# Kernel optimization log

Measured on AMD Instinct MI355X. Metric: run time of the kernel, lower is better.

## Reference

```python
import jax, jax.numpy as jnp
import numpy as np

BS, N, C = 16, 128, 512
EPS = 1e-5


def setup_inputs() -> dict:
    key = jax.random.key(0)
    ks = jax.random.split(key, 6)
    x = jax.random.normal(ks[0], (BS, N, C), dtype=jnp.float32)
    y = jax.random.normal(ks[1], (BS, C), dtype=jnp.float32)
    # edge conv: Conv2d(2C -> 1, 1x1), init std sqrt(2/(1*1*1))
    conv_e_w = jax.random.normal(ks[2], (1, 2 * C), dtype=jnp.float32) * np.sqrt(2.0)
    conv_e_b = jnp.zeros((1,), dtype=jnp.float32)
    bn_e_g = jnp.ones((1,), dtype=jnp.float32)
    bn_e_b = jnp.zeros((1,), dtype=jnp.float32)
    bn_e_m = jnp.zeros((1,), dtype=jnp.float32)
    bn_e_v = jnp.ones((1,), dtype=jnp.float32)
    # feature conv: Conv2d(2C -> C, 1x1), init std sqrt(2/C)
    conv_f_w = jax.random.normal(ks[3], (C, 2 * C), dtype=jnp.float32) * np.sqrt(2.0 / C)
    conv_f_b = jnp.zeros((C,), dtype=jnp.float32)
    bn_f_g = jnp.ones((C,), dtype=jnp.float32)
    bn_f_b = jnp.zeros((C,), dtype=jnp.float32)
    bn_f_m = jnp.zeros((C,), dtype=jnp.float32)
    bn_f_v = jnp.ones((C,), dtype=jnp.float32)
    return {
        "x": x, "y": y,
        "conv_e_w": conv_e_w, "conv_e_b": conv_e_b,
        "bn_e_g": bn_e_g, "bn_e_b": bn_e_b, "bn_e_m": bn_e_m, "bn_e_v": bn_e_v,
        "conv_f_w": conv_f_w, "conv_f_b": conv_f_b,
        "bn_f_g": bn_f_g, "bn_f_b": bn_f_b, "bn_f_m": bn_f_m, "bn_f_v": bn_f_v,
    }


def reference(x, y, conv_e_w, conv_e_b, bn_e_g, bn_e_b, bn_e_m, bn_e_v,
              conv_f_w, conv_f_b, bn_f_g, bn_f_b, bn_f_m, bn_f_v):
    bs, n, c = x.shape
    # ---- Wcompute: pairwise |x_i - x_j| -> conv1x1(2C->1) + BN + mask + softmax ----
    diff = jnp.abs(x[:, :, None, :] - x[:, None, :, :])  # [bs, N, N, C]
    w_diff = conv_e_w[0, :c]   # weights on pairwise-diff channels
    w_y = conv_e_w[0, c:]      # weights on broadcast y channels
    # 1x1 conv collapses to einsum; y part is constant over (i, j)
    score = (jnp.einsum('bijc,c->bij', diff, w_diff)
             + (y @ w_y)[:, None, None] + conv_e_b[0])  # [bs, N, N]
    # BatchNorm2d(1), inference mode
    score = (score - bn_e_m[0]) * (bn_e_g[0] * jax.lax.rsqrt(bn_e_v[0] + EPS)) + bn_e_b[0]
    # mask diagonal (W_id * 1e8) then softmax over neighbors j
    score = score - jnp.eye(n, dtype=score.dtype)[None] * 1e8
    W = jax.nn.softmax(score, axis=2)  # [bs, N, N]
    # ---- Gconv: neighbor aggregation + conv1x1(2C->C) + BN + ReLU ----
    x_nb = jnp.einsum('bij,bjc->bic', W, x)       # [bs, N, C]
    h = jnp.concatenate([x, x_nb], axis=2)        # [bs, N, 2C]
    out = jnp.einsum('bnk,ck->bnc', h, conv_f_w) + conv_f_b  # [bs, N, C]
    # BatchNorm2d(C), inference mode (per-channel)
    out = (out - bn_f_m) * (bn_f_g * jax.lax.rsqrt(bn_f_v + EPS)) + bn_f_b
    return jax.nn.relu(out)
```

## Files before the change

### kernel.cpp

```cpp
#include <hip/hip_runtime.h>
#include <hip/hip_bf16.h>

#define NTOK 128
#define CHN  512
#define KTOT 1024
#define EPSV 1e-5f

typedef __attribute__((ext_vector_type(8))) short bf16x8;
typedef __attribute__((ext_vector_type(4))) float f32x4;

union BfPack4 { ushort4 u; __hip_bfloat16 h[4]; };


__global__ __launch_bounds__(256)
void k0_transpose(const float* __restrict__ xg,
                  float* __restrict__ xT,
                  __hip_bfloat16* __restrict__ xTbf,
                  __hip_bfloat16* __restrict__ hb)
{
    __shared__ float ts[64 * 68];
    const int t  = threadIdx.x;
    const int bk = blockIdx.x;
    const int b  = bk >> 4;
    const int jt = (bk >> 3) & 1;
    const int ct = bk & 7;
    const int j0 = jt * 64, c0 = ct * 64;

    const int jr = t >> 2, qd = t & 3;
    const float* src = xg + ((size_t)(b * NTOK) + j0 + jr) * CHN + c0 + qd * 16;
    float4 v0 = *(const float4*)&src[0];
    float4 v1 = *(const float4*)&src[4];
    float4 v2 = *(const float4*)&src[8];
    float4 v3 = *(const float4*)&src[12];
    *(float4*)&ts[jr * 68 + qd * 16 + 0]  = v0;
    *(float4*)&ts[jr * 68 + qd * 16 + 4]  = v1;
    *(float4*)&ts[jr * 68 + qd * 16 + 8]  = v2;
    *(float4*)&ts[jr * 68 + qd * 16 + 12] = v3;

    {
        __hip_bfloat16* hrow = hb + ((size_t)(b * NTOK) + j0 + jr) * KTOT + c0 + qd * 16;
        BfPack4 p;
        p.h[0]=__float2bfloat16(v0.x); p.h[1]=__float2bfloat16(v0.y);
        p.h[2]=__float2bfloat16(v0.z); p.h[3]=__float2bfloat16(v0.w);
        *(ushort4*)&hrow[0] = p.u;
        p.h[0]=__float2bfloat16(v1.x); p.h[1]=__float2bfloat16(v1.y);
        p.h[2]=__float2bfloat16(v1.z); p.h[3]=__float2bfloat16(v1.w);
        *(ushort4*)&hrow[4] = p.u;
        p.h[0]=__float2bfloat16(v2.x); p.h[1]=__float2bfloat16(v2.y);
        p.h[2]=__float2bfloat16(v2.z); p.h[3]=__float2bfloat16(v2.w);
        *(ushort4*)&hrow[8] = p.u;
        p.h[0]=__float2bfloat16(v3.x); p.h[1]=__float2bfloat16(v3.y);
        p.h[2]=__float2bfloat16(v3.z); p.h[3]=__float2bfloat16(v3.w);
        *(ushort4*)&hrow[12] = p.u;
    }
    __syncthreads();

    const int cs = t >> 4, jj = (t & 15) * 4;
    #pragma unroll
    for (int m = 0; m < 4; ++m) {
        const int c = cs + 16 * m;
        float4 o;
        o.x = ts[(jj + 0) * 68 + c];
        o.y = ts[(jj + 1) * 68 + c];
        o.z = ts[(jj + 2) * 68 + c];
        o.w = ts[(jj + 3) * 68 + c];
        const size_t base = ((size_t)(b * CHN) + c0 + c) * NTOK + j0 + jj;
        *(float4*)&xT[base] = o;
        BfPack4 p;
        p.h[0]=__float2bfloat16(o.x); p.h[1]=__float2bfloat16(o.y);
        p.h[2]=__float2bfloat16(o.z); p.h[3]=__float2bfloat16(o.w);
        *(ushort4*)&xTbf[base] = p.u;
    }
}

__global__ __launch_bounds__(128)
void k1a_scores(const float* __restrict__ xg,
                const float* __restrict__ xT,
                const float* __restrict__ wde,
                float* __restrict__ part)
{
    const int bk = blockIdx.x;
    const int s  = bk & 7;
    const int iq = (bk >> 3) & 31;
    const int b  = bk >> 8;
    const int i0 = iq * 4;
    const int c0 = s * 64;
    const int j  = threadIdx.x;

    const float* xtp = xT + ((size_t)(b * CHN) + c0) * NTOK + j;
    const float* xip = xg + ((size_t)(b * NTOK) + i0) * CHN + c0;

    float acc0 = 0.f, acc1 = 0.f, acc2 = 0.f, acc3 = 0.f;

    #pragma unroll 2
    for (int cc = 0; cc < 64; cc += 8) {
        float xj[8];
        #pragma unroll
        for (int k = 0; k < 8; ++k) xj[k] = xtp[(cc + k) * NTOK];
        #pragma unroll
        for (int k = 0; k < 8; ++k) {
            const int c = cc + k;
            const float wd  = wde[c0 + c];
            const float xi0 = xip[0 * CHN + c];
            const float xi1 = xip[1 * CHN + c];
            const float xi2 = xip[2 * CHN + c];
            const float xi3 = xip[3 * CHN + c];
            acc0 += fabsf(xi0 - xj[k]) * wd;
            acc1 += fabsf(xi1 - xj[k]) * wd;
            acc2 += fabsf(xi2 - xj[k]) * wd;
            acc3 += fabsf(xi3 - xj[k]) * wd;
        }
    }

    float* pp = part + ((size_t)s * 16 + b) * (NTOK * NTOK) + (size_t)i0 * NTOK + j;
    pp[0 * NTOK] = acc0;
    pp[1 * NTOK] = acc1;
    pp[2 * NTOK] = acc2;
    pp[3 * NTOK] = acc3;
}

__global__ __launch_bounds__(128)
void k1b_softmax(const float* __restrict__ part,
                 const float* __restrict__ bn_e_g,
                 const float* __restrict__ bn_e_v,
                 __hip_bfloat16* __restrict__ Wbf)
{
    const int bk = blockIdx.x;
    const int b  = bk >> 6;
    const int i  = (bk & 63) * 2 + (threadIdx.x >> 6);
    const int l  = threadIdx.x & 63;

    const float* pp = part + (size_t)(b * NTOK + i) * NTOK;
    float p1 = 0.f, p2 = 0.f;
    #pragma unroll
    for (int s = 0; s < 8; ++s) {
        p1 += pp[(size_t)s * 16 * NTOK * NTOK + l];
        p2 += pp[(size_t)s * 16 * NTOK * NTOK + l + 64];
    }
    const float sc = bn_e_g[0] * rsqrtf(bn_e_v[0] + EPSV);
    float l1 = p1 * sc - (l == i ? 1e8f : 0.f);
    float l2 = p2 * sc - (l + 64 == i ? 1e8f : 0.f);

    float m = fmaxf(l1, l2);
    #pragma unroll
    for (int off = 32; off > 0; off >>= 1) m = fmaxf(m, __shfl_xor(m, off));
    const float e1 = __expf(l1 - m);
    const float e2 = __expf(l2 - m);
    float ssum = e1 + e2;
    #pragma unroll
    for (int off = 32; off > 0; off >>= 1) ssum += __shfl_xor(ssum, off);
    const float inv = 1.f / ssum;

    __hip_bfloat16* wr = Wbf + (size_t)(b * NTOK + i) * NTOK;
    wr[l]      = __float2bfloat16(e1 * inv);
    wr[l + 64] = __float2bfloat16(e2 * inv);
}

__global__ __launch_bounds__(256)
void k1c_xnb(const __hip_bfloat16* __restrict__ Wbf,
             const __hip_bfloat16* __restrict__ xTbf,
             const float* __restrict__ wf,
             __hip_bfloat16* __restrict__ hb,
             __hip_bfloat16* __restrict__ wfb)
{
    const int bk = blockIdx.x;
    const int t  = threadIdx.x;

    {
        const float* wr = wf + (size_t)bk * KTOT;
        float4 u = *(const float4*)&wr[t * 4];
        BfPack4 p;
        p.h[0]=__float2bfloat16(u.x); p.h[1]=__float2bfloat16(u.y);
        p.h[2]=__float2bfloat16(u.z); p.h[3]=__float2bfloat16(u.w);
        *(ushort4*)&wfb[(size_t)bk * KTOT + t * 4] = p.u;
    }

    const int b  = bk >> 5;
    const int mt = (bk >> 3) & 3;
    const int ct = bk & 7;
    const int i0 = mt * 32, c0 = ct * 64;

    const int w    = t >> 6;
    const int lane = t & 63;
    const int wm   = w & 1;
    const int wn   = w >> 1;
    const int m16  = lane & 15;
    const int q    = lane >> 4;

    const short* A0 = (const short*)Wbf  + (size_t)(b * NTOK + i0 + wm * 16 + m16) * NTOK + q * 8;
    const short* B0 = (const short*)xTbf + ((size_t)(b * CHN) + c0 + wn * 32 + m16) * NTOK + q * 8;

    f32x4 acc0 = {0.f, 0.f, 0.f, 0.f};
    f32x4 acc1 = acc0;

    #pragma unroll
    for (int k0 = 0; k0 < NTOK; k0 += 32) {
        const bf16x8 a  = *(const bf16x8*)(A0 + k0);
        const bf16x8 b0 = *(const bf16x8*)(B0 + k0);
        const bf16x8 b1 = *(const bf16x8*)(B0 + 16 * NTOK + k0);
        acc0 = __builtin_amdgcn_mfma_f32_16x16x32_bf16(a, b0, acc0, 0, 0, 0);
        acc1 = __builtin_amdgcn_mfma_f32_16x16x32_bf16(a, b1, acc1, 0, 0, 0);
    }

    #pragma unroll
    for (int ni = 0; ni < 2; ++ni) {
        const int c = c0 + wn * 32 + ni * 16 + m16;
        const f32x4 ac = ni ? acc1 : acc0;
        #pragma unroll
        for (int r = 0; r < 4; ++r) {
            const int i = i0 + wm * 16 + q * 4 + r;
            hb[(size_t)(b * NTOK + i) * KTOT + CHN + c] = __float2bfloat16(ac[r]);
        }
    }
}

__global__ __launch_bounds__(256)
void k2_gemm_bn_relu(const __hip_bfloat16* __restrict__ hbp,
                     const __hip_bfloat16* __restrict__ wfbp,
                     const float* __restrict__ fb,
                     const float* __restrict__ gg,
                     const float* __restrict__ bb,
                     const float* __restrict__ mm,
                     const float* __restrict__ vv,
                     float* __restrict__ out)
{
    const int blk  = blockIdx.x;
    const int r0   = (blk >> 3) << 6;
    const int c0   = (blk & 7) << 6;
    const int t    = threadIdx.x;
    const int w    = t >> 6;
    const int lane = t & 63;
    const int wm   = w & 1;
    const int wn   = w >> 1;
    const int m16  = lane & 15;
    const int qq   = lane >> 4;

    const short* A0 = (const short*)hbp  + (size_t)(r0 + wm * 32 + m16) * KTOT + qq * 8;
    const short* B0 = (const short*)wfbp + (size_t)(c0 + wn * 32 + m16) * KTOT + qq * 8;

    f32x4 acc00 = {0.f, 0.f, 0.f, 0.f};
    f32x4 acc01 = acc00, acc10 = acc00, acc11 = acc00;

    #pragma unroll 4
    for (int k0 = 0; k0 < KTOT; k0 += 32) {
        const bf16x8 aA = *(const bf16x8*)(A0 + k0);
        const bf16x8 aB = *(const bf16x8*)(A0 + 16 * KTOT + k0);
        const bf16x8 bA = *(const bf16x8*)(B0 + k0);
        const bf16x8 bB = *(const bf16x8*)(B0 + 16 * KTOT + k0);
        acc00 = __builtin_amdgcn_mfma_f32_16x16x32_bf16(aA, bA, acc00, 0, 0, 0);
        acc01 = __builtin_amdgcn_mfma_f32_16x16x32_bf16(aA, bB, acc01, 0, 0, 0);
        acc10 = __builtin_amdgcn_mfma_f32_16x16x32_bf16(aB, bA, acc10, 0, 0, 0);
        acc11 = __builtin_amdgcn_mfma_f32_16x16x32_bf16(aB, bB, acc11, 0, 0, 0);
    }

    #pragma unroll
    for (int ni = 0; ni < 2; ++ni) {
        const int c = c0 + wn * 32 + ni * 16 + m16;
        const float gf = gg[c] * rsqrtf(vv[c] + EPSV);
        const float ad = fb[c] - mm[c];
        const float bv = bb[c];
        const f32x4 acr0 = ni ? acc01 : acc00;
        const f32x4 acr1 = ni ? acc11 : acc10;
        #pragma unroll
        for (int r2 = 0; r2 < 4; ++r2) {
            int row = r0 + wm * 32 + qq * 4 + r2;
            float val = (acr0[r2] + ad) * gf + bv;
            out[(size_t)row * CHN + c] = fmaxf(val, 0.f);
            row += 16;
            val = (acr1[r2] + ad) * gf + bv;
            out[(size_t)row * CHN + c] = fmaxf(val, 0.f);
        }
    }
}

extern "C" void kernel_launch(void* const* d_in, const int* in_sizes, int n_in,
                              void* d_out, int out_size, void* d_ws, size_t ws_size,
                              hipStream_t stream) {
    const float* x        = (const float*)d_in[0];
    const float* conv_e_w = (const float*)d_in[2];
    const float* bn_e_g   = (const float*)d_in[4];
    const float* bn_e_v   = (const float*)d_in[7];
    const float* conv_f_w = (const float*)d_in[8];
    const float* conv_f_b = (const float*)d_in[9];
    const float* bn_f_g   = (const float*)d_in[10];
    const float* bn_f_b   = (const float*)d_in[11];
    const float* bn_f_m   = (const float*)d_in[12];
    const float* bn_f_v   = (const float*)d_in[13];
    float* out = (float*)d_out;

    char* ws = (char*)d_ws;
    float*           xT   = (float*)(ws);
    float*           part = (float*)(ws + (4u << 20));
    __hip_bfloat16*  hb   = (__hip_bfloat16*)(ws + (12u << 20));
    __hip_bfloat16*  wfb  = (__hip_bfloat16*)(ws + (16u << 20));
    __hip_bfloat16*  Wbf  = (__hip_bfloat16*)(ws + (17u << 20));
    __hip_bfloat16*  xTbf = (__hip_bfloat16*)(ws + (17u << 20) + (512u << 10));

    k0_transpose<<<256, 256, 0, stream>>>(x, xT, xTbf, hb);
    k1a_scores<<<4096, 128, 0, stream>>>(x, xT, conv_e_w, part);
    k1b_softmax<<<1024, 128, 0, stream>>>(part, bn_e_g, bn_e_v, Wbf);
    k1c_xnb<<<512, 256, 0, stream>>>(Wbf, xTbf, conv_f_w, hb, wfb);
    k2_gemm_bn_relu<<<256, 256, 0, stream>>>(hb, wfb, conv_f_b, bn_f_g, bn_f_b,
                                             bn_f_m, bn_f_v, out);
}
```

Measured before the change: 124.3 us.

## Fuse pairwise scores, softmax and neighbor aggregation into one kernel

Merges the score, softmax and x_nb MFMA kernels into one 512-thread kernel per (batch, 8-row) tile. Partial scores are reduced in LDS rather than written to and re-read from a global partial buffer, and the softmax weights stay in LDS for the MFMA. The weight bf16 conversion moves into the transpose kernel. This removes two launches and the global round-trips, but the grid shrinks from 4096 blocks to 256 and half of each MFMA tile is zero padding.

```diff
diff --git a/kernel.cpp b/kernel.cpp
--- a/kernel.cpp
+++ b/kernel.cpp
@@ -16,7 +16,9 @@
 void k0_transpose(const float* __restrict__ xg,
                   float* __restrict__ xT,
                   __hip_bfloat16* __restrict__ xTbf,
-                  __hip_bfloat16* __restrict__ hb)
+                  __hip_bfloat16* __restrict__ hb,
+                  const float* __restrict__ wf,
+                  __hip_bfloat16* __restrict__ wfb)
 {
     __shared__ float ts[64 * 68];
     const int t  = threadIdx.x;
@@ -52,6 +54,21 @@
         p.h[0]=__float2bfloat16(v3.x); p.h[1]=__float2bfloat16(v3.y);
         p.h[2]=__float2bfloat16(v3.z); p.h[3]=__float2bfloat16(v3.w);
         *(ushort4*)&hrow[12] = p.u;
+    }
+
+    {
+        const int r   = 2 * bk + (t >> 7);
+        const int col = (t & 127) * 8;
+        const float* wsrc = wf + (size_t)r * KTOT + col;
+        float4 u0 = *(const float4*)&wsrc[0];
+        float4 u1 = *(const float4*)&wsrc[4];
+        BfPack4 p;
+        p.h[0]=__float2bfloat16(u0.x); p.h[1]=__float2bfloat16(u0.y);
+        p.h[2]=__float2bfloat16(u0.z); p.h[3]=__float2bfloat16(u0.w);
+        *(ushort4*)&wfb[(size_t)r * KTOT + col] = p.u;
+        p.h[0]=__float2bfloat16(u1.x); p.h[1]=__float2bfloat16(u1.y);
+        p.h[2]=__float2bfloat16(u1.z); p.h[3]=__float2bfloat16(u1.w);
+        *(ushort4*)&wfb[(size_t)r * KTOT + col + 4] = p.u;
     }
     __syncthreads();
 
@@ -73,143 +90,111 @@
     }
 }
 
-__global__ __launch_bounds__(128)
-void k1a_scores(const float* __restrict__ xg,
-                const float* __restrict__ xT,
-                const float* __restrict__ wde,
-                float* __restrict__ part)
+__global__ __launch_bounds__(512)
+void k1_fused(const float* __restrict__ xg,
+              const float* __restrict__ xT,
+              const float* __restrict__ wde,
+              const float* __restrict__ bn_e_g,
+              const float* __restrict__ bn_e_v,
+              const __hip_bfloat16* __restrict__ xTbf,
+              __hip_bfloat16* __restrict__ hb)
 {
+    __shared__ float        pLDS[4][8][128];
+    __shared__ __hip_bfloat16 Wlds[16][136];
+
+    const int t  = threadIdx.x;
+    const int w  = t >> 6;
+    const int l  = t & 63;
     const int bk = blockIdx.x;
-    const int s  = bk & 7;
-    const int iq = (bk >> 3) & 31;
-    const int b  = bk >> 8;
-    const int i0 = iq * 4;
-    const int c0 = s * 64;
-    const int j  = threadIdx.x;
-
-    const float* xtp = xT + ((size_t)(b * CHN) + c0) * NTOK + j;
-    const float* xip = xg + ((size_t)(b * NTOK) + i0) * CHN + c0;
-
-    float acc0 = 0.f, acc1 = 0.f, acc2 = 0.f, acc3 = 0.f;
-
-    #pragma unroll 2
-    for (int cc = 0; cc < 64; cc += 8) {
-        float xj[8];
-        #pragma unroll
-        for (int k = 0; k < 8; ++k) xj[k] = xtp[(cc + k) * NTOK];
-        #pragma unroll
-        for (int k = 0; k < 8; ++k) {
-            const int c = cc + k;
-            const float wd  = wde[c0 + c];
+    const int b  = bk >> 4;
+    const int i0 = (bk & 15) * 8;
+
+    {
+        const int rp = __builtin_amdgcn_readfirstlane(w >> 2);
+        const int cq = __builtin_amdgcn_readfirstlane(w & 3);
+        const int c0 = cq * 128;
+        const int r0 = rp * 4;
+
+        const float* __restrict__ xtp = xT + ((size_t)(b * CHN) + c0) * NTOK + l;
+        const float* __restrict__ xip = xg + ((size_t)(b * NTOK) + i0 + r0) * CHN + c0;
+        const float* __restrict__ wdp = wde + c0;
+
+        float a00=0.f,a01=0.f,a10=0.f,a11=0.f,a20=0.f,a21=0.f,a30=0.f,a31=0.f;
+        #pragma unroll 8
+        for (int c = 0; c < 128; ++c) {
+            const float xj1 = xtp[c * NTOK];
+            const float xj2 = xtp[c * NTOK + 64];
+            const float wd  = wdp[c];
             const float xi0 = xip[0 * CHN + c];
             const float xi1 = xip[1 * CHN + c];
             const float xi2 = xip[2 * CHN + c];
             const float xi3 = xip[3 * CHN + c];
-            acc0 += fabsf(xi0 - xj[k]) * wd;
-            acc1 += fabsf(xi1 - xj[k]) * wd;
-            acc2 += fabsf(xi2 - xj[k]) * wd;
-            acc3 += fabsf(xi3 - xj[k]) * wd;
+            a00 += fabsf(xi0 - xj1) * wd;  a01 += fabsf(xi0 - xj2) * wd;
+            a10 += fabsf(xi1 - xj1) * wd;  a11 += fabsf(xi1 - xj2) * wd;
+            a20 += fabsf(xi2 - xj1) * wd;  a21 += fabsf(xi2 - xj2) * wd;
+            a30 += fabsf(xi3 - xj1) * wd;  a31 += fabsf(xi3 - xj2) * wd;
         }
-    }
-
-    float* pp = part + ((size_t)s * 16 + b) * (NTOK * NTOK) + (size_t)i0 * NTOK + j;
-    pp[0 * NTOK] = acc0;
-    pp[1 * NTOK] = acc1;
-    pp[2 * NTOK] = acc2;
-    pp[3 * NTOK] = acc3;
-}
-
-__global__ __launch_bounds__(128)
-void k1b_softmax(const float* __restrict__ part,
-                 const float* __restrict__ bn_e_g,
-                 const float* __restrict__ bn_e_v,
-                 __hip_bfloat16* __restrict__ Wbf)
-{
-    const int bk = blockIdx.x;
-    const int b  = bk >> 6;
-    const int i  = (bk & 63) * 2 + (threadIdx.x >> 6);
-    const int l  = threadIdx.x & 63;
-
-    const float* pp = part + (size_t)(b * NTOK + i) * NTOK;
-    float p1 = 0.f, p2 = 0.f;
-    #pragma unroll
-    for (int s = 0; s < 8; ++s) {
-        p1 += pp[(size_t)s * 16 * NTOK * NTOK + l];
-        p2 += pp[(size_t)s * 16 * NTOK * NTOK + l + 64];
-    }
-    const float sc = bn_e_g[0] * rsqrtf(bn_e_v[0] + EPSV);
-    float l1 = p1 * sc - (l == i ? 1e8f : 0.f);
-    float l2 = p2 * sc - (l + 64 == i ? 1e8f : 0.f);
-
-    float m = fmaxf(l1, l2);
-    #pragma unroll
-    for (int off = 32; off > 0; off >>= 1) m = fmaxf(m, __shfl_xor(m, off));
-    const float e1 = __expf(l1 - m);
-    const float e2 = __expf(l2 - m);
-    float ssum = e1 + e2;
-    #pragma unroll
-    for (int off = 32; off > 0; off >>= 1) ssum += __shfl_xor(ssum, off);
-    const float inv = 1.f / ssum;
-
-    __hip_bfloat16* wr = Wbf + (size_t)(b * NTOK + i) * NTOK;
-    wr[l]      = __float2bfloat16(e1 * inv);
-    wr[l + 64] = __float2bfloat16(e2 * inv);
-}
-
-__global__ __launch_bounds__(256)
-void k1c_xnb(const __hip_bfloat16* __restrict__ Wbf,
-             const __hip_bfloat16* __restrict__ xTbf,
-             const float* __restrict__ wf,
-             __hip_bfloat16* __restrict__ hb,
-             __hip_bfloat16* __restrict__ wfb)
-{
-    const int bk = blockIdx.x;
-    const int t  = threadIdx.x;
-
-    {
-        const float* wr = wf + (size_t)bk * KTOT;
-        float4 u = *(const float4*)&wr[t * 4];
-        BfPack4 p;
-        p.h[0]=__float2bfloat16(u.x); p.h[1]=__float2bfloat16(u.y);
-        p.h[2]=__float2bfloat16(u.z); p.h[3]=__float2bfloat16(u.w);
-        *(ushort4*)&wfb[(size_t)bk * KTOT + t * 4] = p.u;
-    }
-
-    const int b  = bk >> 5;
-    const int mt = (bk >> 3) & 3;
-    const int ct = bk & 7;
-    const int i0 = mt * 32, c0 = ct * 64;
-
-    const int w    = t >> 6;
-    const int lane = t & 63;
-    const int wm   = w & 1;
-    const int wn   = w >> 1;
-    const int m16  = lane & 15;
-    const int q    = lane >> 4;
-
-    const short* A0 = (const short*)Wbf  + (size_t)(b * NTOK + i0 + wm * 16 + m16) * NTOK + q * 8;
-    const short* B0 = (const short*)xTbf + ((size_t)(b * CHN) + c0 + wn * 32 + m16) * NTOK + q * 8;
-
-    f32x4 acc0 = {0.f, 0.f, 0.f, 0.f};
-    f32x4 acc1 = acc0;
-
-    #pragma unroll
-    for (int k0 = 0; k0 < NTOK; k0 += 32) {
-        const bf16x8 a  = *(const bf16x8*)(A0 + k0);
-        const bf16x8 b0 = *(const bf16x8*)(B0 + k0);
-        const bf16x8 b1 = *(const bf16x8*)(B0 + 16 * NTOK + k0);
-        acc0 = __builtin_amdgcn_mfma_f32_16x16x32_bf16(a, b0, acc0, 0, 0, 0);
-        acc1 = __builtin_amdgcn_mfma_f32_16x16x32_bf16(a, b1, acc1, 0, 0, 0);
-    }
-
-    #pragma unroll
-    for (int ni = 0; ni < 2; ++ni) {
-        const int c = c0 + wn * 32 + ni * 16 + m16;
-        const f32x4 ac = ni ? acc1 : acc0;
-        #pragma unroll
-        for (int r = 0; r < 4; ++r) {
-            const int i = i0 + wm * 16 + q * 4 + r;
-            hb[(size_t)(b * NTOK + i) * KTOT + CHN + c] = __float2bfloat16(ac[r]);
+        pLDS[cq][r0 + 0][l] = a00;  pLDS[cq][r0 + 0][l + 64] = a01;
+        pLDS[cq][r0 + 1][l] = a10;  pLDS[cq][r0 + 1][l + 64] = a11;
+        pLDS[cq][r0 + 2][l] = a20;  pLDS[cq][r0 + 2][l + 64] = a21;
+        pLDS[cq][r0 + 3][l] = a30;  pLDS[cq][r0 + 3][l + 64] = a31;
+    }
+    __syncthreads();
+
+    {
+        float p1 = pLDS[0][w][l]      + pLDS[1][w][l]
+                 + pLDS[2][w][l]      + pLDS[3][w][l];
+        float p2 = pLDS[0][w][l + 64] + pLDS[1][w][l + 64]
+                 + pLDS[2][w][l + 64] + pLDS[3][w][l + 64];
+        const float sc = bn_e_g[0] * rsqrtf(bn_e_v[0] + EPSV);
+        const int ir = i0 + w;
+        float l1 = p1 * sc - (l == ir ? 1e8f : 0.f);
+        float l2 = p2 * sc - (l + 64 == ir ? 1e8f : 0.f);
+
+        float m = fmaxf(l1, l2);
+        #pragma unroll
+        for (int off = 32; off > 0; off >>= 1) m = fmaxf(m, __shfl_xor(m, off));
+        const float e1 = __expf(l1 - m);
+        const float e2 = __expf(l2 - m);
+        float ssum = e1 + e2;
+        #pragma unroll
+        for (int off = 32; off > 0; off >>= 1) ssum += __shfl_xor(ssum, off);
+        const float inv = 1.f / ssum;
+
+        Wlds[w][l]          = __float2bfloat16(e1 * inv);
+        Wlds[w][l + 64]     = __float2bfloat16(e2 * inv);
+        Wlds[w + 8][l]      = __float2bfloat16(0.f);
+        Wlds[w + 8][l + 64] = __float2bfloat16(0.f);
+    }
+    __syncthreads();
+
+    {
+        const int m16 = l & 15;
+        const int q   = l >> 4;
+
+        bf16x8 afr[4];
+        #pragma unroll
+        for (int kk = 0; kk < 4; ++kk)
+            afr[kk] = *(const bf16x8*)&Wlds[m16][q * 8 + kk * 32];
+
+        const int cbase = w * 64;
+        #pragma unroll
+        for (int ni = 0; ni < 4; ++ni) {
+            const int c = cbase + ni * 16 + m16;
+            const short* B0 = (const short*)xTbf + ((size_t)(b * CHN) + c) * NTOK + q * 8;
+            f32x4 acc = {0.f, 0.f, 0.f, 0.f};
+            #pragma unroll
+            for (int kk = 0; kk < 4; ++kk) {
+                const bf16x8 bfr = *(const bf16x8*)(B0 + kk * 32);
+                acc = __builtin_amdgcn_mfma_f32_16x16x32_bf16(afr[kk], bfr, acc, 0, 0, 0);
+            }
+            if (q < 2) {
+                #pragma unroll
+                for (int r = 0; r < 4; ++r) {
+                    const int i = i0 + q * 4 + r;
+                    hb[(size_t)(b * NTOK + i) * KTOT + CHN + c] = __float2bfloat16(acc[r]);
+                }
+            }
         }
     }
 }
@@ -290,16 +275,12 @@
 
     char* ws = (char*)d_ws;
     float*           xT   = (float*)(ws);
-    float*           part = (float*)(ws + (4u << 20));
     __hip_bfloat16*  hb   = (__hip_bfloat16*)(ws + (12u << 20));
     __hip_bfloat16*  wfb  = (__hip_bfloat16*)(ws + (16u << 20));
-    __hip_bfloat16*  Wbf  = (__hip_bfloat16*)(ws + (17u << 20));
     __hip_bfloat16*  xTbf = (__hip_bfloat16*)(ws + (17u << 20) + (512u << 10));
 
-    k0_transpose<<<256, 256, 0, stream>>>(x, xT, xTbf, hb);
-    k1a_scores<<<4096, 128, 0, stream>>>(x, xT, conv_e_w, part);
-    k1b_softmax<<<1024, 128, 0, stream>>>(part, bn_e_g, bn_e_v, Wbf);
-    k1c_xnb<<<512, 256, 0, stream>>>(Wbf, xTbf, conv_f_w, hb, wfb);
+    k0_transpose<<<256, 256, 0, stream>>>(x, xT, xTbf, hb, conv_f_w, wfb);
+    k1_fused<<<256, 512, 0, stream>>>(x, xT, conv_e_w, bn_e_g, bn_e_v, xTbf, hb);
     k2_gemm_bn_relu<<<256, 256, 0, stream>>>(hb, wfb, conv_f_b, bn_f_g, bn_f_b,
                                              bn_f_m, bn_f_v, out);
 }
```

After: 120.4 us. 3.2% less time.
